# Performance work log

Measured on AMD Instinct MI355X. Metric: run time of the kernel, lower is better.

The kernel has to match this reference:

```python
import jax, jax.numpy as jnp
import numpy as np

B, D, H1, H2, E, O = 32768, 256, 512, 256, 16, 64


def setup_inputs() -> dict:
    key = jax.random.key(0)
    ks = jax.random.split(key, 12)
    s = lambda fan_in: 1.0 / np.sqrt(fan_in)
    return {
        "x": jax.random.normal(ks[0], (B, D), dtype=jnp.float32),
        "gate_w": jax.random.normal(ks[1], (D, E), dtype=jnp.float32) * s(D),
        "gate_b": jnp.zeros((E,), dtype=jnp.float32),
        "W1": jax.random.normal(ks[2], (E, D, H1), dtype=jnp.float32) * s(D),
        "b1": jnp.zeros((E, H1), dtype=jnp.float32),
        "W2": jax.random.normal(ks[3], (E, H1, H2), dtype=jnp.float32) * s(H1),
        "b2": jnp.zeros((E, H2), dtype=jnp.float32),
        "W3": jax.random.normal(ks[4], (E, H2, O), dtype=jnp.float32) * s(H2),
        "b3": jnp.zeros((E, O), dtype=jnp.float32),
        "head_w": jax.random.normal(ks[5], (O, 1), dtype=jnp.float32) * s(O),
        "head_b": jnp.zeros((1,), dtype=jnp.float32),
    }


def reference(x, gate_w, gate_b, W1, b1, W2, b2, W3, b3, head_w, head_b):
    # gating: softmax over experts, [B, E]
    gates = jax.nn.softmax(x @ gate_w + gate_b, axis=-1)
    # all-expert dense MLP as batched GEMMs over leading expert axis
    h1 = jax.nn.relu(jnp.einsum('bd,edh->ebh', x, W1) + b1[:, None, :])   # [E,B,H1]
    h2 = jax.nn.relu(jnp.einsum('ebh,ehk->ebk', h1, W2) + b2[:, None, :])  # [E,B,H2]
    eo = jnp.einsum('ebk,eko->ebo', h2, W3) + b3[:, None, :]               # [E,B,O]
    # gated combination: sum_e gates[b,e] * eo[e,b,:]
    fused = jnp.einsum('be,ebo->bo', gates, eo)                            # [B,O]
    yts = (fused @ head_w + head_b)[:, 0]                                  # [B]
    return yts
```

## Files before the change

### kernel.cpp

```cpp
#include <hip/hip_runtime.h>

#define B_TOK 32768
#define D_IN  256
#define H1D   512
#define H2D   256
#define NE    16
#define NO    64

typedef _Float16 half8 __attribute__((ext_vector_type(8)));
typedef _Float16 half4 __attribute__((ext_vector_type(4)));
typedef float   float4_t __attribute__((ext_vector_type(4)));

__global__ void prep_kernel(const float* __restrict__ W1, const float* __restrict__ W2,
                            const float* __restrict__ W3, const float* __restrict__ b3,
                            const float* __restrict__ hw, const float* __restrict__ gw,
                            _Float16* __restrict__ w1p, _Float16* __restrict__ w2p,
                            float* __restrict__ w3h, float* __restrict__ c3,
                            _Float16* __restrict__ gwp) {
  int blk = blockIdx.x;
  int tid = threadIdx.x;
  if (blk < 1024) {
    int t = blk * 256 + tid;
    int lane = t & 63;
    int kt   = (t >> 6) & 7;
    int ntg  = (t >> 9) & 31;
    int e    = t >> 14;
    int n  = ntg * 16 + (lane & 15);
    int kb = kt * 32 + (lane >> 4) * 8;
    half8 v;
    #pragma unroll
    for (int j = 0; j < 8; ++j)
      v[j] = (_Float16)W1[((size_t)(e * D_IN + kb + j)) * H1D + n];
    *(half8*)(w1p + (size_t)t * 8) = v;
  } else if (blk < 2048) {
    int t = (blk - 1024) * 256 + tid;
    int lane = t & 63;
    int ktg  = (t >> 6) & 15;
    int ntg  = (t >> 10) & 15;
    int e    = t >> 14;
    int n  = ntg * 16 + (lane & 15);
    int kb = ktg * 32 + (lane >> 4) * 8;
    half8 v;
    #pragma unroll
    for (int j = 0; j < 8; ++j)
      v[j] = (_Float16)W2[((size_t)(e * H1D + kb + j)) * H2D + n];
    *(half8*)(w2p + (size_t)t * 8) = v;
  } else if (blk < 2065) {
    int t = (blk - 2048) * 256 + tid;
    if (t < NE * H2D) {
      int e = t >> 8, h = t & 255;
      float s = 0.f;
      #pragma unroll
      for (int o = 0; o < NO; ++o) s = fmaf(W3[((size_t)(e * H2D + h)) * NO + o], hw[o], s);
      w3h[t] = s;
    } else if (t < NE * H2D + NE) {
      int e = t - NE * H2D;
      float s = 0.f;
      #pragma unroll
      for (int o = 0; o < NO; ++o) s = fmaf(b3[e * NO + o], hw[o], s);
      c3[e] = s;
    }
  } else {
    for (int t = tid; t < 512; t += 256) {
      int lane = t & 63;
      int kt   = t >> 6;
      int e  = lane & 15;
      int kb = kt * 32 + (lane >> 4) * 8;
      half8 v;
      #pragma unroll
      for (int j = 0; j < 8; ++j)
        v[j] = (_Float16)gw[(kb + j) * NE + e];
      *(half8*)(gwp + (size_t)t * 8) = v;
    }
  }
}

__global__ __launch_bounds__(256, 2) void moe_main(
    const float* __restrict__ x,
    const float* __restrict__ b1,
    const float* __restrict__ b2,
    const _Float16* __restrict__ w1p,
    const _Float16* __restrict__ w2p,
    const _Float16* __restrict__ gwp,
    const float* __restrict__ gb,
    const float* __restrict__ w3h,
    const float* __restrict__ c3,
    const float* __restrict__ head_b,
    float* __restrict__ out) {
  __shared__ _Float16 x_lds[32 * 512];
  __shared__ _Float16 h1c[32 * 512];
  __shared__ float g_lds[64 * 17];
  __shared__ float fin[4 * 64];

  const int tid  = threadIdx.x;
  const int w    = tid >> 6;
  const int lane = tid & 63;
  const int q    = lane >> 4;
  const int l16  = lane & 15;
  const int m0   = blockIdx.x * 64;

  #pragma unroll
  for (int f = 0; f < 8; ++f) {
    const float* xr = x + (size_t)(m0 + w * 16 + l16) * D_IN + f * 32 + q * 8;
    float4_t v0 = *(const float4_t*)(xr);
    float4_t v1 = *(const float4_t*)(xr + 4);
    half8 h;
    h[0] = (_Float16)v0[0]; h[1] = (_Float16)v0[1];
    h[2] = (_Float16)v0[2]; h[3] = (_Float16)v0[3];
    h[4] = (_Float16)v1[0]; h[5] = (_Float16)v1[1];
    h[6] = (_Float16)v1[2]; h[7] = (_Float16)v1[3];
    *(half8*)(x_lds + (size_t)(w * 8 + f) * 512 + lane * 8) = h;
  }
  __syncthreads();

  {
    float gbv = gb[l16];
    float4_t lg = (float4_t){0.f, 0.f, 0.f, 0.f};
    #pragma unroll
    for (int kt = 0; kt < 8; ++kt) {
      half8 xa = *(const half8*)(x_lds + (size_t)(w * 8 + kt) * 512 + lane * 8);
      half8 bfr = *(const half8*)(gwp + (size_t)kt * 512 + lane * 8);
      lg = __builtin_amdgcn_mfma_f32_16x16x32_f16(xa, bfr, lg, 0, 0, 0);
    }
    #pragma unroll
    for (int r = 0; r < 4; ++r) {
      float v = lg[r] + gbv;
      float m = v;
      m = fmaxf(m, __shfl_xor(m, 1));
      m = fmaxf(m, __shfl_xor(m, 2));
      m = fmaxf(m, __shfl_xor(m, 4));
      m = fmaxf(m, __shfl_xor(m, 8));
      float p = __expf(v - m);
      float s = p;
      s += __shfl_xor(s, 1);
      s += __shfl_xor(s, 2);
      s += __shfl_xor(s, 4);
      s += __shfl_xor(s, 8);
      g_lds[(w * 16 + q * 4 + r) * 17 + l16] = p / s;
    }
  }

  float yacc[4][4];
  #pragma unroll
  for (int mt = 0; mt < 4; ++mt)
    #pragma unroll
    for (int r = 0; r < 4; ++r) yacc[mt][r] = 0.f;

  for (int e = 0; e < NE; ++e) {
    float4_t h2[4][4];
    #pragma unroll
    for (int mt = 0; mt < 4; ++mt)
      #pragma unroll
      for (int nt = 0; nt < 4; ++nt)
        h2[mt][nt] = (float4_t){0.f, 0.f, 0.f, 0.f};

    #pragma unroll
    for (int ch = 0; ch < 2; ++ch) {
      float4_t a1[4][4];
      #pragma unroll
      for (int mt = 0; mt < 4; ++mt)
        #pragma unroll
        for (int nt = 0; nt < 4; ++nt)
          a1[mt][nt] = (float4_t){0.f, 0.f, 0.f, 0.f};

      const _Float16* w1e =
          w1p + ((size_t)((e * 32 + ch * 16 + w * 4) * 8)) * 512 + lane * 8;
      #pragma unroll
      for (int kt = 0; kt < 8; ++kt) {
        half8 wc[4];
        #pragma unroll
        for (int mt = 0; mt < 4; ++mt)
          wc[mt] = *(const half8*)(w1e + (size_t)(mt * 8 + kt) * 512);
        half8 xb[4];
        #pragma unroll
        for (int nt = 0; nt < 4; ++nt)
          xb[nt] = *(const half8*)(x_lds + (size_t)(nt * 8 + kt) * 512 + lane * 8);
        #pragma unroll
        for (int mt = 0; mt < 4; ++mt)
          #pragma unroll
          for (int nt = 0; nt < 4; ++nt)
            a1[mt][nt] = __builtin_amdgcn_mfma_f32_16x16x32_f16(
                wc[mt], xb[nt], a1[mt][nt], 0, 0, 0);
      }

      #pragma unroll
      for (int mt = 0; mt < 4; ++mt) {
        int colbase = ch * 256 + (w * 4 + mt) * 16 + q * 4;
        float4_t bb = *(const float4_t*)(b1 + e * H1D + colbase);
        int qp = ((mt & 1) << 1) + (q >> 1);
        int fo = (qp * 16 + l16) * 8 + ((q & 1) << 2);
        #pragma unroll
        for (int nt = 0; nt < 4; ++nt) {
          half4 hv;
          #pragma unroll
          for (int r = 0; r < 4; ++r)
            hv[r] = (_Float16)fmaxf(a1[mt][nt][r] + bb[r], 0.f);
          *(half4*)(h1c + (size_t)(nt * 8 + w * 2 + (mt >> 1)) * 512 + fo) = hv;
        }
      }

      __syncthreads();

      const _Float16* w2e =
          w2p + ((size_t)((e * 16 + w * 4) * 16 + ch * 8)) * 512 + lane * 8;
      #pragma unroll
      for (int kt = 0; kt < 8; ++kt) {
        half8 w2c[4];
        #pragma unroll
        for (int nt = 0; nt < 4; ++nt)
          w2c[nt] = *(const half8*)(w2e + (size_t)(nt * 16 + kt) * 512);
        half8 hac[4];
        #pragma unroll
        for (int mt = 0; mt < 4; ++mt)
          hac[mt] = *(const half8*)(h1c + (size_t)(mt * 8 + kt) * 512 + lane * 8);
        #pragma unroll
        for (int mt = 0; mt < 4; ++mt)
          #pragma unroll
          for (int nt = 0; nt < 4; ++nt)
            h2[mt][nt] = __builtin_amdgcn_mfma_f32_16x16x32_f16(
                hac[mt], w2c[nt], h2[mt][nt], 0, 0, 0);
      }

      __syncthreads();
    }

    float b2v[4], w3v[4];
    #pragma unroll
    for (int nt = 0; nt < 4; ++nt) {
      int n = w * 64 + nt * 16 + l16;
      b2v[nt] = b2[e * H2D + n];
      w3v[nt] = w3h[e * H2D + n];
    }
    #pragma unroll
    for (int mt = 0; mt < 4; ++mt) {
      #pragma unroll
      for (int r = 0; r < 4; ++r) {
        float s = 0.f;
        #pragma unroll
        for (int nt = 0; nt < 4; ++nt)
          s += fmaxf(h2[mt][nt][r] + b2v[nt], 0.f) * w3v[nt];
        yacc[mt][r] += g_lds[(mt * 16 + q * 4 + r) * 17 + e] * s;
      }
    }
  }

  #pragma unroll
  for (int mt = 0; mt < 4; ++mt) {
    #pragma unroll
    for (int r = 0; r < 4; ++r) {
      float v = yacc[mt][r];
      v += __shfl_xor(v, 1);
      v += __shfl_xor(v, 2);
      v += __shfl_xor(v, 4);
      v += __shfl_xor(v, 8);
      yacc[mt][r] = v;
    }
  }
  if (l16 == 0) {
    #pragma unroll
    for (int mt = 0; mt < 4; ++mt)
      #pragma unroll
      for (int r = 0; r < 4; ++r)
        fin[w * 64 + mt * 16 + q * 4 + r] = yacc[mt][r];
  }
  __syncthreads();
  if (tid < 64) {
    float sum = fin[tid] + fin[64 + tid] + fin[128 + tid] + fin[192 + tid];
    float gc = 0.f;
    #pragma unroll
    for (int e = 0; e < NE; ++e) gc += g_lds[tid * 17 + e] * c3[e];
    out[m0 + tid] = sum + gc + head_b[0];
  }
}

extern "C" void kernel_launch(void* const* d_in, const int* in_sizes, int n_in,
                              void* d_out, int out_size, void* d_ws, size_t ws_size,
                              hipStream_t stream) {
  const float* x      = (const float*)d_in[0];
  const float* gate_w = (const float*)d_in[1];
  const float* gate_b = (const float*)d_in[2];
  const float* W1     = (const float*)d_in[3];
  const float* b1     = (const float*)d_in[4];
  const float* W2     = (const float*)d_in[5];
  const float* b2     = (const float*)d_in[6];
  const float* W3     = (const float*)d_in[7];
  const float* b3     = (const float*)d_in[8];
  const float* head_w = (const float*)d_in[9];
  const float* head_b = (const float*)d_in[10];
  float* out = (float*)d_out;

  char* ws = (char*)d_ws;
  _Float16* w1p = (_Float16*)(ws);
  _Float16* w2p = (_Float16*)(ws + 4194304);
  _Float16* gwp = (_Float16*)(ws + 8388608);
  float*    w3h = (float*)(ws + 8396800);
  float*    c3  = (float*)(ws + 8413184);

  hipLaunchKernelGGL(prep_kernel, dim3(2066), dim3(256), 0, stream,
                     W1, W2, W3, b3, head_w, gate_w, w1p, w2p, w3h, c3, gwp);
  hipLaunchKernelGGL(moe_main, dim3(B_TOK / 64), dim3(256), 0, stream,
                     x, b1, b2, w1p, w2p, gwp, gate_b, w3h, c3, head_b, out);
}
```

Before: 358.6 us.

## Double token tile to 128 with 8 waves to halve per-token weight traffic

```diff
diff --git a/kernel.cpp b/kernel.cpp
--- a/kernel.cpp
+++ b/kernel.cpp
@@ -6,6 +6,7 @@
 #define H2D   256
 #define NE    16
 #define NO    64
+#define TK    128
 
 typedef _Float16 half8 __attribute__((ext_vector_type(8)));
 typedef _Float16 half4 __attribute__((ext_vector_type(4)));
@@ -75,7 +76,7 @@
   }
 }
 
-__global__ __launch_bounds__(256, 2) void moe_main(
+__global__ __launch_bounds__(512, 2) void moe_main(
     const float* __restrict__ x,
     const float* __restrict__ b1,
     const float* __restrict__ b2,
@@ -87,17 +88,17 @@
     const float* __restrict__ c3,
     const float* __restrict__ head_b,
     float* __restrict__ out) {
-  __shared__ _Float16 x_lds[32 * 512];
-  __shared__ _Float16 h1c[32 * 512];
-  __shared__ float g_lds[64 * 17];
-  __shared__ float fin[4 * 64];
+  __shared__ _Float16 x_lds[64 * 512];
+  __shared__ _Float16 h1c[64 * 512];
+  __shared__ float g_lds[TK * 17];
+  __shared__ float fin[8 * TK];
 
   const int tid  = threadIdx.x;
   const int w    = tid >> 6;
   const int lane = tid & 63;
   const int q    = lane >> 4;
   const int l16  = lane & 15;
-  const int m0   = blockIdx.x * 64;
+  const int m0   = blockIdx.x * TK;
 
   #pragma unroll
   for (int f = 0; f < 8; ++f) {
@@ -140,112 +141,112 @@
     }
   }
 
-  float yacc[4][4];
+  float yacc[8][4];
   #pragma unroll
-  for (int mt = 0; mt < 4; ++mt)
+  for (int mt = 0; mt < 8; ++mt)
     #pragma unroll
     for (int r = 0; r < 4; ++r) yacc[mt][r] = 0.f;
 
   for (int e = 0; e < NE; ++e) {
-    float4_t h2[4][4];
-    #pragma unroll
-    for (int mt = 0; mt < 4; ++mt)
-      #pragma unroll
-      for (int nt = 0; nt < 4; ++nt)
-        h2[mt][nt] = (float4_t){0.f, 0.f, 0.f, 0.f};
+    float4_t h2[8][2];
+    #pragma unroll
+    for (int mt = 0; mt < 8; ++mt)
+      #pragma unroll
+      for (int j = 0; j < 2; ++j)
+        h2[mt][j] = (float4_t){0.f, 0.f, 0.f, 0.f};
 
     #pragma unroll
     for (int ch = 0; ch < 2; ++ch) {
-      float4_t a1[4][4];
-      #pragma unroll
-      for (int mt = 0; mt < 4; ++mt)
-        #pragma unroll
-        for (int nt = 0; nt < 4; ++nt)
-          a1[mt][nt] = (float4_t){0.f, 0.f, 0.f, 0.f};
+      float4_t a1[2][8];
+      #pragma unroll
+      for (int i = 0; i < 2; ++i)
+        #pragma unroll
+        for (int nt = 0; nt < 8; ++nt)
+          a1[i][nt] = (float4_t){0.f, 0.f, 0.f, 0.f};
 
       const _Float16* w1e =
-          w1p + ((size_t)((e * 32 + ch * 16 + w * 4) * 8)) * 512 + lane * 8;
+          w1p + ((size_t)((e * 32 + ch * 16 + w * 2) * 8)) * 512 + lane * 8;
       #pragma unroll
       for (int kt = 0; kt < 8; ++kt) {
-        half8 wc[4];
-        #pragma unroll
-        for (int mt = 0; mt < 4; ++mt)
-          wc[mt] = *(const half8*)(w1e + (size_t)(mt * 8 + kt) * 512);
-        half8 xb[4];
-        #pragma unroll
-        for (int nt = 0; nt < 4; ++nt)
+        half8 wc[2];
+        #pragma unroll
+        for (int i = 0; i < 2; ++i)
+          wc[i] = *(const half8*)(w1e + (size_t)(i * 8 + kt) * 512);
+        half8 xb[8];
+        #pragma unroll
+        for (int nt = 0; nt < 8; ++nt)
           xb[nt] = *(const half8*)(x_lds + (size_t)(nt * 8 + kt) * 512 + lane * 8);
         #pragma unroll
-        for (int mt = 0; mt < 4; ++mt)
+        for (int i = 0; i < 2; ++i)
           #pragma unroll
-          for (int nt = 0; nt < 4; ++nt)
-            a1[mt][nt] = __builtin_amdgcn_mfma_f32_16x16x32_f16(
-                wc[mt], xb[nt], a1[mt][nt], 0, 0, 0);
+          for (int nt = 0; nt < 8; ++nt)
+            a1[i][nt] = __builtin_amdgcn_mfma_f32_16x16x32_f16(
+                wc[i], xb[nt], a1[i][nt], 0, 0, 0);
       }
 
       #pragma unroll
-      for (int mt = 0; mt < 4; ++mt) {
-        int colbase = ch * 256 + (w * 4 + mt) * 16 + q * 4;
+      for (int i = 0; i < 2; ++i) {
+        int colbase = ch * 256 + (w * 2 + i) * 16 + q * 4;
         float4_t bb = *(const float4_t*)(b1 + e * H1D + colbase);
-        int qp = ((mt & 1) << 1) + (q >> 1);
+        int qp = (i << 1) + (q >> 1);
         int fo = (qp * 16 + l16) * 8 + ((q & 1) << 2);
         #pragma unroll
-        for (int nt = 0; nt < 4; ++nt) {
+        for (int nt = 0; nt < 8; ++nt) {
           half4 hv;
           #pragma unroll
           for (int r = 0; r < 4; ++r)
-            hv[r] = (_Float16)fmaxf(a1[mt][nt][r] + bb[r], 0.f);
-          *(half4*)(h1c + (size_t)(nt * 8 + w * 2 + (mt >> 1)) * 512 + fo) = hv;
+            hv[r] = (_Float16)fmaxf(a1[i][nt][r] + bb[r], 0.f);
+          *(half4*)(h1c + (size_t)(nt * 8 + w) * 512 + fo) = hv;
         }
       }
 
       __syncthreads();
 
       const _Float16* w2e =
-          w2p + ((size_t)((e * 16 + w * 4) * 16 + ch * 8)) * 512 + lane * 8;
+          w2p + ((size_t)((e * 16 + w * 2) * 16 + ch * 8)) * 512 + lane * 8;
       #pragma unroll
       for (int kt = 0; kt < 8; ++kt) {
-        half8 w2c[4];
-        #pragma unroll
-        for (int nt = 0; nt < 4; ++nt)
-          w2c[nt] = *(const half8*)(w2e + (size_t)(nt * 16 + kt) * 512);
-        half8 hac[4];
-        #pragma unroll
-        for (int mt = 0; mt < 4; ++mt)
+        half8 w2c[2];
+        #pragma unroll
+        for (int j = 0; j < 2; ++j)
+          w2c[j] = *(const half8*)(w2e + (size_t)(j * 16 + kt) * 512);
+        half8 hac[8];
+        #pragma unroll
+        for (int mt = 0; mt < 8; ++mt)
           hac[mt] = *(const half8*)(h1c + (size_t)(mt * 8 + kt) * 512 + lane * 8);
         #pragma unroll
-        for (int mt = 0; mt < 4; ++mt)
+        for (int mt = 0; mt < 8; ++mt)
           #pragma unroll
-          for (int nt = 0; nt < 4; ++nt)
-            h2[mt][nt] = __builtin_amdgcn_mfma_f32_16x16x32_f16(
-                hac[mt], w2c[nt], h2[mt][nt], 0, 0, 0);
+          for (int j = 0; j < 2; ++j)
+            h2[mt][j] = __builtin_amdgcn_mfma_f32_16x16x32_f16(
+                hac[mt], w2c[j], h2[mt][j], 0, 0, 0);
       }
 
       __syncthreads();
     }
 
-    float b2v[4], w3v[4];
-    #pragma unroll
-    for (int nt = 0; nt < 4; ++nt) {
-      int n = w * 64 + nt * 16 + l16;
-      b2v[nt] = b2[e * H2D + n];
-      w3v[nt] = w3h[e * H2D + n];
-    }
-    #pragma unroll
-    for (int mt = 0; mt < 4; ++mt) {
+    float b2v[2], w3v[2];
+    #pragma unroll
+    for (int j = 0; j < 2; ++j) {
+      int n = (w * 2 + j) * 16 + l16;
+      b2v[j] = b2[e * H2D + n];
+      w3v[j] = w3h[e * H2D + n];
+    }
+    #pragma unroll
+    for (int mt = 0; mt < 8; ++mt) {
       #pragma unroll
       for (int r = 0; r < 4; ++r) {
         float s = 0.f;
         #pragma unroll
-        for (int nt = 0; nt < 4; ++nt)
-          s += fmaxf(h2[mt][nt][r] + b2v[nt], 0.f) * w3v[nt];
+        for (int j = 0; j < 2; ++j)
+          s += fmaxf(h2[mt][j][r] + b2v[j], 0.f) * w3v[j];
         yacc[mt][r] += g_lds[(mt * 16 + q * 4 + r) * 17 + e] * s;
       }
     }
   }
 
   #pragma unroll
-  for (int mt = 0; mt < 4; ++mt) {
+  for (int mt = 0; mt < 8; ++mt) {
     #pragma unroll
     for (int r = 0; r < 4; ++r) {
       float v = yacc[mt][r];
@@ -258,14 +259,16 @@
   }
   if (l16 == 0) {
     #pragma unroll
-    for (int mt = 0; mt < 4; ++mt)
+    for (int mt = 0; mt < 8; ++mt)
       #pragma unroll
       for (int r = 0; r < 4; ++r)
-        fin[w * 64 + mt * 16 + q * 4 + r] = yacc[mt][r];
+        fin[w * TK + mt * 16 + q * 4 + r] = yacc[mt][r];
   }
   __syncthreads();
-  if (tid < 64) {
-    float sum = fin[tid] + fin[64 + tid] + fin[128 + tid] + fin[192 + tid];
+  if (tid < TK) {
+    float sum = 0.f;
+    #pragma unroll
+    for (int k = 0; k < 8; ++k) sum += fin[k * TK + tid];
     float gc = 0.f;
     #pragma unroll
     for (int e = 0; e < NE; ++e) gc += g_lds[tid * 17 + e] * c3[e];
@@ -298,6 +301,6 @@
 
   hipLaunchKernelGGL(prep_kernel, dim3(2066), dim3(256), 0, stream,
                      W1, W2, W3, b3, head_w, gate_w, w1p, w2p, w3h, c3, gwp);
-  hipLaunchKernelGGL(moe_main, dim3(B_TOK / 64), dim3(256), 0, stream,
+  hipLaunchKernelGGL(moe_main, dim3(B_TOK / TK), dim3(512), 0, stream,
                      x, b1, b2, w1p, w2p, gwp, gate_b, w3h, c3, head_b, out);
 }
```

After: 344.0 us. 1.04x faster.

## Switch expert GEMMs to 32x32x16 MFMA with repacked weight and activation layouts

Applied to the files above, without the earlier changes.

```diff
diff --git a/kernel.cpp b/kernel.cpp
--- a/kernel.cpp
+++ b/kernel.cpp
@@ -9,7 +9,9 @@
 
 typedef _Float16 half8 __attribute__((ext_vector_type(8)));
 typedef _Float16 half4 __attribute__((ext_vector_type(4)));
-typedef float   float4_t __attribute__((ext_vector_type(4)));
+typedef float   float4_t  __attribute__((ext_vector_type(4)));
+typedef float   float16_t __attribute__((ext_vector_type(16)));
+
 
 __global__ void prep_kernel(const float* __restrict__ W1, const float* __restrict__ W2,
                             const float* __restrict__ W3, const float* __restrict__ b3,
@@ -22,28 +24,28 @@
   if (blk < 1024) {
     int t = blk * 256 + tid;
     int lane = t & 63;
-    int kt   = (t >> 6) & 7;
-    int ntg  = (t >> 9) & 31;
+    int kd   = (t >> 6) & 15;
+    int ct   = (t >> 10) & 15;
     int e    = t >> 14;
-    int n  = ntg * 16 + (lane & 15);
-    int kb = kt * 32 + (lane >> 4) * 8;
+    int m  = ct * 32 + (lane & 31);
+    int d0 = kd * 16 + (lane >> 5) * 8;
     half8 v;
     #pragma unroll
     for (int j = 0; j < 8; ++j)
-      v[j] = (_Float16)W1[((size_t)(e * D_IN + kb + j)) * H1D + n];
+      v[j] = (_Float16)W1[((size_t)(e * D_IN + d0 + j)) * H1D + m];
     *(half8*)(w1p + (size_t)t * 8) = v;
   } else if (blk < 2048) {
     int t = (blk - 1024) * 256 + tid;
     int lane = t & 63;
-    int ktg  = (t >> 6) & 15;
-    int ntg  = (t >> 10) & 15;
+    int kcg  = (t >> 6) & 31;
+    int nc   = (t >> 11) & 7;
     int e    = t >> 14;
-    int n  = ntg * 16 + (lane & 15);
-    int kb = ktg * 32 + (lane >> 4) * 8;
+    int n  = nc * 32 + (lane & 31);
+    int k0 = kcg * 16 + (lane >> 5) * 8;
     half8 v;
     #pragma unroll
     for (int j = 0; j < 8; ++j)
-      v[j] = (_Float16)W2[((size_t)(e * H1D + kb + j)) * H2D + n];
+      v[j] = (_Float16)W2[((size_t)(e * H1D + k0 + j)) * H2D + n];
     *(half8*)(w2p + (size_t)t * 8) = v;
   } else if (blk < 2065) {
     int t = (blk - 2048) * 256 + tid;
@@ -61,15 +63,15 @@
       c3[e] = s;
     }
   } else {
-    for (int t = tid; t < 512; t += 256) {
+    for (int t = tid; t < 1024; t += 256) {
       int lane = t & 63;
-      int kt   = t >> 6;
-      int e  = lane & 15;
-      int kb = kt * 32 + (lane >> 4) * 8;
+      int kd   = t >> 6;
+      int er = lane & 31;
+      int d0 = kd * 16 + (lane >> 5) * 8;
       half8 v;
       #pragma unroll
       for (int j = 0; j < 8; ++j)
-        v[j] = (_Float16)gw[(kb + j) * NE + e];
+        v[j] = (er < NE) ? (_Float16)gw[(d0 + j) * NE + er] : (_Float16)0.f;
       *(half8*)(gwp + (size_t)t * 8) = v;
     }
   }
@@ -95,13 +97,15 @@
   const int tid  = threadIdx.x;
   const int w    = tid >> 6;
   const int lane = tid & 63;
-  const int q    = lane >> 4;
-  const int l16  = lane & 15;
+  const int l31  = lane & 31;
+  const int hl   = lane >> 5;
   const int m0   = blockIdx.x * 64;
 
   #pragma unroll
-  for (int f = 0; f < 8; ++f) {
-    const float* xr = x + (size_t)(m0 + w * 16 + l16) * D_IN + f * 32 + q * 8;
+  for (int i = 0; i < 8; ++i) {
+    int f  = w * 8 + i;
+    int tt = f >> 4, kd = f & 15;
+    const float* xr = x + (size_t)(m0 + tt * 32 + l31) * D_IN + kd * 16 + hl * 8;
     float4_t v0 = *(const float4_t*)(xr);
     float4_t v1 = *(const float4_t*)(xr + 4);
     half8 h;
@@ -109,159 +113,165 @@
     h[2] = (_Float16)v0[2]; h[3] = (_Float16)v0[3];
     h[4] = (_Float16)v1[0]; h[5] = (_Float16)v1[1];
     h[6] = (_Float16)v1[2]; h[7] = (_Float16)v1[3];
-    *(half8*)(x_lds + (size_t)(w * 8 + f) * 512 + lane * 8) = h;
+    *(half8*)(x_lds + (size_t)f * 512 + lane * 8) = h;
   }
   __syncthreads();
 
-  {
-    float gbv = gb[l16];
-    float4_t lg = (float4_t){0.f, 0.f, 0.f, 0.f};
-    #pragma unroll
-    for (int kt = 0; kt < 8; ++kt) {
-      half8 xa = *(const half8*)(x_lds + (size_t)(w * 8 + kt) * 512 + lane * 8);
-      half8 bfr = *(const half8*)(gwp + (size_t)kt * 512 + lane * 8);
-      lg = __builtin_amdgcn_mfma_f32_16x16x32_f16(xa, bfr, lg, 0, 0, 0);
-    }
-    #pragma unroll
-    for (int r = 0; r < 4; ++r) {
-      float v = lg[r] + gbv;
-      float m = v;
-      m = fmaxf(m, __shfl_xor(m, 1));
-      m = fmaxf(m, __shfl_xor(m, 2));
-      m = fmaxf(m, __shfl_xor(m, 4));
-      m = fmaxf(m, __shfl_xor(m, 8));
-      float p = __expf(v - m);
-      float s = p;
-      s += __shfl_xor(s, 1);
-      s += __shfl_xor(s, 2);
-      s += __shfl_xor(s, 4);
-      s += __shfl_xor(s, 8);
-      g_lds[(w * 16 + q * 4 + r) * 17 + l16] = p / s;
-    }
-  }
-
-  float yacc[4][4];
+  if (w < 2) {
+    const int tt = w;
+    float16_t lg;
+    #pragma unroll
+    for (int i = 0; i < 16; ++i) lg[i] = 0.f;
+    #pragma unroll
+    for (int kd = 0; kd < 16; ++kd) {
+      half8 av = *(const half8*)(gwp + (size_t)kd * 512 + lane * 8);
+      half8 xv = *(const half8*)(x_lds + (size_t)(tt * 16 + kd) * 512 + lane * 8);
+      lg = __builtin_amdgcn_mfma_f32_32x32x16_f16(av, xv, lg, 0, 0, 0);
+    }
+    int tok = tt * 32 + l31;
+    #pragma unroll
+    for (int r = 0; r < 8; ++r) {
+      int ee = 4 * hl + (r & 3) + 8 * (r >> 2);
+      g_lds[tok * 17 + ee] = lg[r] + gb[ee];
+    }
+  }
+  __syncthreads();
+  if (tid < 64) {
+    float mx = g_lds[tid * 17];
+    #pragma unroll
+    for (int e = 1; e < NE; ++e) mx = fmaxf(mx, g_lds[tid * 17 + e]);
+    float sm = 0.f;
+    #pragma unroll
+    for (int e = 0; e < NE; ++e) {
+      float p = __expf(g_lds[tid * 17 + e] - mx);
+      g_lds[tid * 17 + e] = p;
+      sm += p;
+    }
+    float inv = 1.f / sm;
+    #pragma unroll
+    for (int e = 0; e < NE; ++e) g_lds[tid * 17 + e] *= inv;
+  }
+
+  float yacc[2][16];
   #pragma unroll
-  for (int mt = 0; mt < 4; ++mt)
-    #pragma unroll
-    for (int r = 0; r < 4; ++r) yacc[mt][r] = 0.f;
+  for (int tt = 0; tt < 2; ++tt)
+    #pragma unroll
+    for (int r = 0; r < 16; ++r) yacc[tt][r] = 0.f;
 
   for (int e = 0; e < NE; ++e) {
-    float4_t h2[4][4];
-    #pragma unroll
-    for (int mt = 0; mt < 4; ++mt)
-      #pragma unroll
-      for (int nt = 0; nt < 4; ++nt)
-        h2[mt][nt] = (float4_t){0.f, 0.f, 0.f, 0.f};
+    float16_t h2[2][2];
+    #pragma unroll
+    for (int tt = 0; tt < 2; ++tt)
+      #pragma unroll
+      for (int ncl = 0; ncl < 2; ++ncl)
+        #pragma unroll
+        for (int i = 0; i < 16; ++i) h2[tt][ncl][i] = 0.f;
 
     #pragma unroll
     for (int ch = 0; ch < 2; ++ch) {
-      float4_t a1[4][4];
-      #pragma unroll
-      for (int mt = 0; mt < 4; ++mt)
-        #pragma unroll
-        for (int nt = 0; nt < 4; ++nt)
-          a1[mt][nt] = (float4_t){0.f, 0.f, 0.f, 0.f};
+      float16_t a1[2][2];
+      #pragma unroll
+      for (int ctl = 0; ctl < 2; ++ctl)
+        #pragma unroll
+        for (int tt = 0; tt < 2; ++tt)
+          #pragma unroll
+          for (int i = 0; i < 16; ++i) a1[ctl][tt][i] = 0.f;
 
       const _Float16* w1e =
-          w1p + ((size_t)((e * 32 + ch * 16 + w * 4) * 8)) * 512 + lane * 8;
-      #pragma unroll
-      for (int kt = 0; kt < 8; ++kt) {
-        half8 wc[4];
-        #pragma unroll
-        for (int mt = 0; mt < 4; ++mt)
-          wc[mt] = *(const half8*)(w1e + (size_t)(mt * 8 + kt) * 512);
-        half8 xb[4];
-        #pragma unroll
-        for (int nt = 0; nt < 4; ++nt)
-          xb[nt] = *(const half8*)(x_lds + (size_t)(nt * 8 + kt) * 512 + lane * 8);
-        #pragma unroll
-        for (int mt = 0; mt < 4; ++mt)
+          w1p + ((size_t)((e * 16 + ch * 8 + w * 2) * 16)) * 512 + lane * 8;
+      #pragma unroll
+      for (int kd = 0; kd < 16; ++kd) {
+        half8 wA[2];
+        wA[0] = *(const half8*)(w1e + (size_t)kd * 512);
+        wA[1] = *(const half8*)(w1e + (size_t)(16 + kd) * 512);
+        half8 xB[2];
+        xB[0] = *(const half8*)(x_lds + (size_t)kd * 512 + lane * 8);
+        xB[1] = *(const half8*)(x_lds + (size_t)(16 + kd) * 512 + lane * 8);
+        #pragma unroll
+        for (int ctl = 0; ctl < 2; ++ctl)
           #pragma unroll
-          for (int nt = 0; nt < 4; ++nt)
-            a1[mt][nt] = __builtin_amdgcn_mfma_f32_16x16x32_f16(
-                wc[mt], xb[nt], a1[mt][nt], 0, 0, 0);
-      }
-
-      #pragma unroll
-      for (int mt = 0; mt < 4; ++mt) {
-        int colbase = ch * 256 + (w * 4 + mt) * 16 + q * 4;
-        float4_t bb = *(const float4_t*)(b1 + e * H1D + colbase);
-        int qp = ((mt & 1) << 1) + (q >> 1);
-        int fo = (qp * 16 + l16) * 8 + ((q & 1) << 2);
-        #pragma unroll
-        for (int nt = 0; nt < 4; ++nt) {
-          half4 hv;
+          for (int tt = 0; tt < 2; ++tt)
+            a1[ctl][tt] = __builtin_amdgcn_mfma_f32_32x32x16_f16(
+                wA[ctl], xB[tt], a1[ctl][tt], 0, 0, 0);
+      }
+
+      #pragma unroll
+      for (int ctl = 0; ctl < 2; ++ctl) {
+        int ct_local = w * 2 + ctl;
+        #pragma unroll
+        for (int g = 0; g < 4; ++g) {
+          int colbase = (ch * 8 + ct_local) * 32 + 8 * g + 4 * hl;
+          float4_t bb = *(const float4_t*)(b1 + e * H1D + colbase);
+          _Float16* dst = h1c + (size_t)(ct_local * 2 + (g >> 1)) * 512 +
+                          (size_t)(l31 + 32 * (g & 1)) * 8 + 4 * hl;
           #pragma unroll
-          for (int r = 0; r < 4; ++r)
-            hv[r] = (_Float16)fmaxf(a1[mt][nt][r] + bb[r], 0.f);
-          *(half4*)(h1c + (size_t)(nt * 8 + w * 2 + (mt >> 1)) * 512 + fo) = hv;
+          for (int tt = 0; tt < 2; ++tt) {
+            half4 hv;
+            #pragma unroll
+            for (int r4 = 0; r4 < 4; ++r4)
+              hv[r4] = (_Float16)fmaxf(a1[ctl][tt][g * 4 + r4] + bb[r4], 0.f);
+            *(half4*)(dst + (size_t)tt * (16 * 512)) = hv;
+          }
         }
       }
 
       __syncthreads();
 
       const _Float16* w2e =
-          w2p + ((size_t)((e * 16 + w * 4) * 16 + ch * 8)) * 512 + lane * 8;
-      #pragma unroll
-      for (int kt = 0; kt < 8; ++kt) {
-        half8 w2c[4];
-        #pragma unroll
-        for (int nt = 0; nt < 4; ++nt)
-          w2c[nt] = *(const half8*)(w2e + (size_t)(nt * 16 + kt) * 512);
-        half8 hac[4];
-        #pragma unroll
-        for (int mt = 0; mt < 4; ++mt)
-          hac[mt] = *(const half8*)(h1c + (size_t)(mt * 8 + kt) * 512 + lane * 8);
-        #pragma unroll
-        for (int mt = 0; mt < 4; ++mt)
+          w2p + ((size_t)((e * 8 + w * 2) * 32 + ch * 16)) * 512 + lane * 8;
+      #pragma unroll
+      for (int kcl = 0; kcl < 16; ++kcl) {
+        half8 wB[2];
+        wB[0] = *(const half8*)(w2e + (size_t)kcl * 512);
+        wB[1] = *(const half8*)(w2e + (size_t)(32 + kcl) * 512);
+        half8 hA[2];
+        hA[0] = *(const half8*)(h1c + (size_t)kcl * 512 + lane * 8);
+        hA[1] = *(const half8*)(h1c + (size_t)(16 + kcl) * 512 + lane * 8);
+        #pragma unroll
+        for (int tt = 0; tt < 2; ++tt)
           #pragma unroll
-          for (int nt = 0; nt < 4; ++nt)
-            h2[mt][nt] = __builtin_amdgcn_mfma_f32_16x16x32_f16(
-                hac[mt], w2c[nt], h2[mt][nt], 0, 0, 0);
+          for (int ncl = 0; ncl < 2; ++ncl)
+            h2[tt][ncl] = __builtin_amdgcn_mfma_f32_32x32x16_f16(
+                hA[tt], wB[ncl], h2[tt][ncl], 0, 0, 0);
       }
 
       __syncthreads();
     }
 
-    float b2v[4], w3v[4];
-    #pragma unroll
-    for (int nt = 0; nt < 4; ++nt) {
-      int n = w * 64 + nt * 16 + l16;
-      b2v[nt] = b2[e * H2D + n];
-      w3v[nt] = w3h[e * H2D + n];
-    }
-    #pragma unroll
-    for (int mt = 0; mt < 4; ++mt) {
-      #pragma unroll
-      for (int r = 0; r < 4; ++r) {
-        float s = 0.f;
-        #pragma unroll
-        for (int nt = 0; nt < 4; ++nt)
-          s += fmaxf(h2[mt][nt][r] + b2v[nt], 0.f) * w3v[nt];
-        yacc[mt][r] += g_lds[(mt * 16 + q * 4 + r) * 17 + e] * s;
+    float b2v[2], w3v[2];
+    #pragma unroll
+    for (int ncl = 0; ncl < 2; ++ncl) {
+      int col = (w * 2 + ncl) * 32 + l31;
+      b2v[ncl] = b2[e * H2D + col];
+      w3v[ncl] = w3h[e * H2D + col];
+    }
+    #pragma unroll
+    for (int tt = 0; tt < 2; ++tt) {
+      #pragma unroll
+      for (int r = 0; r < 16; ++r) {
+        float s = fmaxf(h2[tt][0][r] + b2v[0], 0.f) * w3v[0] +
+                  fmaxf(h2[tt][1][r] + b2v[1], 0.f) * w3v[1];
+        int tok = tt * 32 + 4 * hl + (r & 3) + 8 * (r >> 2);
+        yacc[tt][r] += g_lds[tok * 17 + e] * s;
       }
     }
   }
 
   #pragma unroll
-  for (int mt = 0; mt < 4; ++mt) {
-    #pragma unroll
-    for (int r = 0; r < 4; ++r) {
-      float v = yacc[mt][r];
+  for (int tt = 0; tt < 2; ++tt) {
+    #pragma unroll
+    for (int r = 0; r < 16; ++r) {
+      float v = yacc[tt][r];
       v += __shfl_xor(v, 1);
       v += __shfl_xor(v, 2);
       v += __shfl_xor(v, 4);
       v += __shfl_xor(v, 8);
-      yacc[mt][r] = v;
-    }
-  }
-  if (l16 == 0) {
-    #pragma unroll
-    for (int mt = 0; mt < 4; ++mt)
-      #pragma unroll
-      for (int r = 0; r < 4; ++r)
-        fin[w * 64 + mt * 16 + q * 4 + r] = yacc[mt][r];
+      v += __shfl_xor(v, 16);
+      if (l31 == 0) {
+        int tok = tt * 32 + 4 * hl + (r & 3) + 8 * (r >> 2);
+        fin[w * 64 + tok] = v;
+      }
+    }
   }
   __syncthreads();
   if (tid < 64) {
@@ -293,8 +303,8 @@
   _Float16* w1p = (_Float16*)(ws);
   _Float16* w2p = (_Float16*)(ws + 4194304);
   _Float16* gwp = (_Float16*)(ws + 8388608);
-  float*    w3h = (float*)(ws + 8396800);
-  float*    c3  = (float*)(ws + 8413184);
+  float*    w3h = (float*)(ws + 8404992);
+  float*    c3  = (float*)(ws + 8421376);
 
   hipLaunchKernelGGL(prep_kernel, dim3(2066), dim3(256), 0, stream,
                      W1, W2, W3, b3, head_w, gate_w, w1p, w2p, w3h, c3, gwp);
```

Measured after the change: 451.9 us. 26.0% more time.

## Halve H1 chunk size to shrink LDS and registers for 3 blocks per CU

Applied to the files above, without the earlier changes.

```diff
diff --git a/kernel.cpp b/kernel.cpp
--- a/kernel.cpp
+++ b/kernel.cpp
@@ -75,7 +75,7 @@
   }
 }
 
-__global__ __launch_bounds__(256, 2) void moe_main(
+__global__ __launch_bounds__(256, 3) void moe_main(
     const float* __restrict__ x,
     const float* __restrict__ b1,
     const float* __restrict__ b2,
@@ -88,9 +88,10 @@
     const float* __restrict__ head_b,
     float* __restrict__ out) {
   __shared__ _Float16 x_lds[32 * 512];
-  __shared__ _Float16 h1c[32 * 512];
-  __shared__ float g_lds[64 * 17];
-  __shared__ float fin[4 * 64];
+  __shared__ _Float16 h1c[16 * 512];
+  __shared__ float g_lds[64 * 16];
+
+  float* fin = (float*)h1c;
 
   const int tid  = threadIdx.x;
   const int w    = tid >> 6;
@@ -136,7 +137,7 @@
       s += __shfl_xor(s, 2);
       s += __shfl_xor(s, 4);
       s += __shfl_xor(s, 8);
-      g_lds[(w * 16 + q * 4 + r) * 17 + l16] = p / s;
+      g_lds[(w * 16 + q * 4 + r) * 16 + l16] = p / s;
     }
   }
 
@@ -155,56 +156,55 @@
         h2[mt][nt] = (float4_t){0.f, 0.f, 0.f, 0.f};
 
     #pragma unroll
-    for (int ch = 0; ch < 2; ++ch) {
-      float4_t a1[4][4];
-      #pragma unroll
-      for (int mt = 0; mt < 4; ++mt)
+    for (int c = 0; c < 4; ++c) {
+      float4_t a1[2][4];
+      #pragma unroll
+      for (int i = 0; i < 2; ++i)
         #pragma unroll
         for (int nt = 0; nt < 4; ++nt)
-          a1[mt][nt] = (float4_t){0.f, 0.f, 0.f, 0.f};
+          a1[i][nt] = (float4_t){0.f, 0.f, 0.f, 0.f};
 
       const _Float16* w1e =
-          w1p + ((size_t)((e * 32 + ch * 16 + w * 4) * 8)) * 512 + lane * 8;
+          w1p + ((size_t)((e * 32 + c * 8 + w * 2) * 8)) * 512 + lane * 8;
       #pragma unroll
       for (int kt = 0; kt < 8; ++kt) {
-        half8 wc[4];
-        #pragma unroll
-        for (int mt = 0; mt < 4; ++mt)
-          wc[mt] = *(const half8*)(w1e + (size_t)(mt * 8 + kt) * 512);
+        half8 wc[2];
+        wc[0] = *(const half8*)(w1e + (size_t)kt * 512);
+        wc[1] = *(const half8*)(w1e + (size_t)(8 + kt) * 512);
         half8 xb[4];
         #pragma unroll
         for (int nt = 0; nt < 4; ++nt)
           xb[nt] = *(const half8*)(x_lds + (size_t)(nt * 8 + kt) * 512 + lane * 8);
         #pragma unroll
-        for (int mt = 0; mt < 4; ++mt)
+        for (int i = 0; i < 2; ++i)
           #pragma unroll
           for (int nt = 0; nt < 4; ++nt)
-            a1[mt][nt] = __builtin_amdgcn_mfma_f32_16x16x32_f16(
-                wc[mt], xb[nt], a1[mt][nt], 0, 0, 0);
+            a1[i][nt] = __builtin_amdgcn_mfma_f32_16x16x32_f16(
+                wc[i], xb[nt], a1[i][nt], 0, 0, 0);
       }
 
       #pragma unroll
-      for (int mt = 0; mt < 4; ++mt) {
-        int colbase = ch * 256 + (w * 4 + mt) * 16 + q * 4;
+      for (int i = 0; i < 2; ++i) {
+        int colbase = c * 128 + (w * 2 + i) * 16 + q * 4;
         float4_t bb = *(const float4_t*)(b1 + e * H1D + colbase);
-        int qp = ((mt & 1) << 1) + (q >> 1);
+        int qp = (i << 1) + (q >> 1);
         int fo = (qp * 16 + l16) * 8 + ((q & 1) << 2);
         #pragma unroll
         for (int nt = 0; nt < 4; ++nt) {
           half4 hv;
           #pragma unroll
           for (int r = 0; r < 4; ++r)
-            hv[r] = (_Float16)fmaxf(a1[mt][nt][r] + bb[r], 0.f);
-          *(half4*)(h1c + (size_t)(nt * 8 + w * 2 + (mt >> 1)) * 512 + fo) = hv;
+            hv[r] = (_Float16)fmaxf(a1[i][nt][r] + bb[r], 0.f);
+          *(half4*)(h1c + (size_t)(nt * 4 + w) * 512 + fo) = hv;
         }
       }
 
       __syncthreads();
 
       const _Float16* w2e =
-          w2p + ((size_t)((e * 16 + w * 4) * 16 + ch * 8)) * 512 + lane * 8;
-      #pragma unroll
-      for (int kt = 0; kt < 8; ++kt) {
+          w2p + ((size_t)((e * 16 + w * 4) * 16 + c * 4)) * 512 + lane * 8;
+      #pragma unroll
+      for (int kt = 0; kt < 4; ++kt) {
         half8 w2c[4];
         #pragma unroll
         for (int nt = 0; nt < 4; ++nt)
@@ -212,7 +212,7 @@
         half8 hac[4];
         #pragma unroll
         for (int mt = 0; mt < 4; ++mt)
-          hac[mt] = *(const half8*)(h1c + (size_t)(mt * 8 + kt) * 512 + lane * 8);
+          hac[mt] = *(const half8*)(h1c + (size_t)(mt * 4 + kt) * 512 + lane * 8);
         #pragma unroll
         for (int mt = 0; mt < 4; ++mt)
           #pragma unroll
@@ -239,7 +239,7 @@
         #pragma unroll
         for (int nt = 0; nt < 4; ++nt)
           s += fmaxf(h2[mt][nt][r] + b2v[nt], 0.f) * w3v[nt];
-        yacc[mt][r] += g_lds[(mt * 16 + q * 4 + r) * 17 + e] * s;
+        yacc[mt][r] += g_lds[(mt * 16 + q * 4 + r) * 16 + e] * s;
       }
     }
   }
@@ -268,7 +268,7 @@
     float sum = fin[tid] + fin[64 + tid] + fin[128 + tid] + fin[192 + tid];
     float gc = 0.f;
     #pragma unroll
-    for (int e = 0; e < NE; ++e) gc += g_lds[tid * 17 + e] * c3[e];
+    for (int e = 0; e < NE; ++e) gc += g_lds[tid * 16 + e] * c3[e];
     out[m0 + tid] = sum + gc + head_b[0];
   }
 }
```

New measurement: 431.3 us. 20.3% more time.
